# Performance work log

Hardware: AMD Instinct MI355X
Metric: run time of the kernel (lower is better)

Reference implementation:

```python
import jax, jax.numpy as jnp
import numpy as np

HEADS = 8


def setup_inputs() -> dict:
    key = jax.random.key(0)
    ks = jax.random.split(key, 6)
    dim = 256
    s = 0.02
    return {
        "x": jax.random.normal(ks[0], (8, dim, 32, 32), jnp.float32),
        "w_qkv": jax.random.normal(ks[1], (3 * dim, dim), jnp.float32) * s,
        "w_out": jax.random.normal(ks[2], (dim, dim), jnp.float32) * s,
        "b_out": jnp.zeros((dim,), jnp.float32),
        "w_g1": jax.random.normal(ks[3], (dim // 4, dim), jnp.float32) * s,
        "b_g1": jnp.zeros((dim // 4,), jnp.float32),
        "w_g2": jax.random.normal(ks[4], (1, dim // 4), jnp.float32) * s,
        "b_g2": jnp.zeros((1,), jnp.float32),
    }


def _conv1x1(t, w, bias=None):
    # 1x1 conv == channel matmul
    y = jnp.einsum('bchw,oc->bohw', t, w)
    if bias is not None:
        y = y + bias[None, :, None, None]
    return y


def _forward(x, w_qkv, w_out, b_out, w_g1, b_g1, w_g2, b_g2):
    b, c, h, w = x.shape
    heads = HEADS
    d = c // heads
    n = h * w
    m = min(h, w)
    scale = d ** (-0.5)

    qkv = _conv1x1(x, w_qkv)  # [b, 3c, h, w]

    def to_heads(t):  # 'b (h d) x y -> b h (x y) d'
        return t.reshape(b, heads, d, n).transpose(0, 1, 3, 2)

    q, k, v = (to_heads(t) for t in jnp.split(qkv, 3, axis=1))

    attn = jax.nn.softmax(jnp.einsum('bhid,bhjd->bhij', q, k) * scale, axis=-1)

    # diagonal branch (anti-diagonal scores are computed in the original but
    # never used in the output -> omitted as dead code)
    q2d = q.reshape(b, heads, h, w, d)
    k2d = k.reshape(b, heads, h, w, d)
    q_dm = jnp.diagonal(q2d, axis1=2, axis2=3)  # [b, heads, d, m]
    k_dm = jnp.diagonal(k2d, axis1=2, axis2=3)
    diag_main = jnp.einsum('bhnd,bhmd->bhnm', q_dm, k_dm) * scale  # [b, heads, d, d]
    diag_vec = jnp.diagonal(diag_main.mean(axis=1), axis1=-2, axis2=-1)  # [b, d]
    diag_vec = jnp.pad(diag_vec, ((0, 0), (0, n - m)))  # [b, n] (d == m)

    DIAG_WEIGHT = 0.3
    enhanced = attn + DIAG_WEIGHT * diag_vec[:, None, :, None]

    out = jnp.einsum('bhij,bhjd->bhid', enhanced, v)  # [b, heads, n, d]
    out = out.reshape(b, heads, h, w, d).transpose(0, 1, 4, 2, 3).reshape(b, c, h, w)

    # left/right asymmetry gate
    mid = w // 2
    left = x[:, :, :, :mid]
    right = x[:, :, :, mid:]
    asym = jnp.abs(left - right[:, :, :, ::-1])  # [b, c, h, w/2]
    # adaptive_avg_pool2d (h, w/2) -> (h, w) with even w == width repeat by 2
    pooled = jnp.repeat(asym, 2, axis=3)
    g = _conv1x1(pooled, w_g1, b_g1)
    g = jax.nn.gelu(g, approximate=False)
    g = jax.nn.sigmoid(_conv1x1(g, w_g2, b_g2))  # [b, 1, h, w]

    out = out * (1.0 + g)
    return _conv1x1(out, w_out, b_out)


def reference(x, w_qkv, w_out, b_out, w_g1, b_g1, w_g2, b_g2):
    return _forward(x, w_qkv, w_out, b_out, w_g1, b_g1, w_g2, b_g2)
```

## Files before the change

### kernel.cpp

```cpp
#include <hip/hip_runtime.h>
#include <hip/hip_bf16.h>
#include <math.h>

#define B 8
#define C 256
#define HEADS 8
#define D 32
#define NPIX 1024
#define OC 768
#define SCALE 0.17677669529663687f
#define LOG2E 1.4426950408889634f

typedef unsigned int uint;
typedef unsigned short u16;
typedef __attribute__((ext_vector_type(8))) short bf16x8;
typedef __attribute__((ext_vector_type(4))) short bf16x4;
typedef __attribute__((ext_vector_type(4))) float f32x4;

static __device__ inline u16 f2bf(float f) {
  uint u = __float_as_uint(f);
  return (u16)((u + 0x7fffu + ((u >> 16) & 1u)) >> 16);
}
static __device__ inline float bfval(u16 v) { return __uint_as_float((uint)v << 16); }
static __device__ inline float bf_lo(uint u) { return __uint_as_float(u << 16); }
static __device__ inline float bf_hi(uint u) { return __uint_as_float(u & 0xffff0000u); }

static __device__ inline uint pk2(float lo, float hi) {
  union { __hip_bfloat162 h; uint u; } cv;
  cv.h = __float22bfloat162_rn(float2{lo, hi});
  return cv.u;
}

__global__ __launch_bounds__(256) void k_prep_gate(
    const float* __restrict__ x, const float* __restrict__ wqkv,
    const float* __restrict__ wout,
    const float* __restrict__ wg1, const float* __restrict__ bg1,
    const float* __restrict__ wg2, const float* __restrict__ bg2,
    u16* __restrict__ WQ, u16* __restrict__ WO, u16* __restrict__ XT,
    float* __restrict__ gate) {
  const int bid = blockIdx.x, t = threadIdx.x;
  __shared__ float smem[16 * 257 + 16 * 65];
  if (bid < 256) {
    const float* src;
    u16* dst;
    int base;
    if (bid < 192) { src = wqkv; dst = WQ; base = bid * 1024; }
    else           { src = wout; dst = WO; base = (bid - 192) * 1024; }
    float4 v = *(const float4*)(src + base + t * 4);
    uint2 pk = make_uint2((uint)f2bf(v.x) | ((uint)f2bf(v.y) << 16),
                          (uint)f2bf(v.z) | ((uint)f2bf(v.w) << 16));
    *(uint2*)(dst + base + t * 4) = pk;
    return;
  }
  if (bid < 768) {
    u16 (*tile)[65] = (u16(*)[65])smem;
    const int id = bid - 256;
    const int pt = id & 15, ct = (id >> 4) & 3, b = id >> 6;
    {
      const int px = t & 63, cq = t >> 6;
      const float* xb = x + ((size_t)(b * C + ct * 64)) * NPIX + pt * 64;
#pragma unroll
      for (int m = 0; m < 16; ++m) {
        const int c = cq * 16 + m;
        tile[c][px] = f2bf(xb[(size_t)c * NPIX + px]);
      }
    }
    __syncthreads();
    {
      const int cc = t & 63, pq = t >> 6;
      const int c = ct * 64 + cc;
      const int kc = c >> 5, quad = (c >> 3) & 3, mm = c & 7;
      u16* dst = XT + ((size_t)((b * 64 + pt * 4 + pq) * 8 + kc) * 512 +
                       quad * 128 + mm);
#pragma unroll
      for (int m = 0; m < 16; ++m)
        dst[m * 8] = tile[cc][pq * 16 + m];
    }
    return;
  }
  const int id = bid - 768;
  const int h = id & 31, b = id >> 5;
  float* pl = smem;
  float* gl = smem + 16 * 257;
  {
    const int c = t;
    const float* row = x + ((size_t)(b * C + c) * NPIX + h * 32);
    float v[32];
#pragma unroll
    for (int m = 0; m < 32; ++m) v[m] = row[m];
#pragma unroll
    for (int k = 0; k < 16; ++k) pl[k * 257 + c] = fabsf(v[k] - v[31 - k]);
  }
  __syncthreads();

  const int o16 = t >> 4, k = t & 15;
#pragma unroll 1
  for (int p = 0; p < 4; ++p) {
    const int o = p * 16 + o16;
    const float* wr = wg1 + o * C;
    float a0 = 0.f, a1 = 0.f, a2 = 0.f, a3 = 0.f;
#pragma unroll 4
    for (int c = 0; c < C; c += 4) {
      a0 += wr[c]     * pl[k * 257 + c];
      a1 += wr[c + 1] * pl[k * 257 + c + 1];
      a2 += wr[c + 2] * pl[k * 257 + c + 2];
      a3 += wr[c + 3] * pl[k * 257 + c + 3];
    }
    float a = bg1[o] + ((a0 + a1) + (a2 + a3));
    gl[k * 65 + o] = 0.5f * a * (1.f + erff(a * 0.70710678118654752f));
  }
  __syncthreads();

  if (t < 16) {
    float s = bg2[0];
    for (int o = 0; o < 64; ++o)
      s += wg2[o] * gl[t * 65 + o];
    gate[(b * 32 + h) * 16 + t] = 1.f / (1.f + expf(-s));
  }
}

__global__ __launch_bounds__(256) void k_qkv_mfma(
    const u16* __restrict__ XTF, const u16* __restrict__ WQ,
    u16* __restrict__ Q, u16* __restrict__ Kk, u16* __restrict__ VT) {
  const int ob = blockIdx.x, pb = blockIdx.y, b = blockIdx.z;
  const int wv = threadIdx.x >> 6, lane = threadIdx.x & 63;
  const int quad = lane >> 4, l15 = lane & 15;
  const int part = ob >> 2;
  const int odl = (ob & 3) * 64 + wv * 16;
  const int hh = odl >> 5, d0 = odl & 31;
  const int bh = b * HEADS + hh;
  const int pix0 = pb * 128;

  const u16* arow = WQ + (size_t)(ob * 64 + wv * 16 + l15) * C;
  bf16x8 af[8];
#pragma unroll
  for (int kc = 0; kc < 8; ++kc)
    af[kc] = *(const bf16x8*)(arow + kc * 32 + quad * 8);

  const u16* xb = XTF + (size_t)(b * 64 + pb * 8) * 8 * 512 + lane * 8;
  f32x4 acc[8];
#pragma unroll
  for (int nt = 0; nt < 8; ++nt) acc[nt] = (f32x4){0.f, 0.f, 0.f, 0.f};

  for (int kc = 0; kc < 8; ++kc) {
#pragma unroll
    for (int nt = 0; nt < 8; ++nt) {
      bf16x8 bfr = *(const bf16x8*)(xb + (size_t)(nt * 8 + kc) * 512);
      acc[nt] = __builtin_amdgcn_mfma_f32_16x16x32_bf16(af[kc], bfr, acc[nt], 0, 0, 0);
    }
  }

  if (part == 0) {
    const float qs = SCALE * LOG2E;
    u16* dst = Q + (size_t)bh * NPIX * D;
#pragma unroll
    for (int nt = 0; nt < 8; ++nt) {
      const int pix = pix0 + nt * 16 + l15;
      uint2 pk = make_uint2(
          (uint)f2bf(acc[nt][0] * qs) | ((uint)f2bf(acc[nt][1] * qs) << 16),
          (uint)f2bf(acc[nt][2] * qs) | ((uint)f2bf(acc[nt][3] * qs) << 16));
      *(uint2*)(dst + (size_t)pix * D + d0 + 4 * quad) = pk;
    }
  } else if (part == 1) {
    u16* kfb = Kk + (size_t)bh * NPIX * D;
    const int lane_k8 = (((d0 >> 3) + (quad >> 1)) * 16 + l15) * 8 + (quad & 1) * 4;
#pragma unroll
    for (int nt = 0; nt < 8; ++nt) {
      uint2 pk = make_uint2(
          (uint)f2bf(acc[nt][0]) | ((uint)f2bf(acc[nt][1]) << 16),
          (uint)f2bf(acc[nt][2]) | ((uint)f2bf(acc[nt][3]) << 16));
      *(uint2*)(kfb + (size_t)(pb * 8 + nt) * 512 + lane_k8) = pk;
    }
  } else {
    u16* vb = VT + (size_t)bh * NPIX * D;
#pragma unroll
    for (int nt = 0; nt < 8; ++nt) {
      const int pix = pix0 + nt * 16 + l15;
      const int jb16 = pix >> 4, qa = (pix >> 2) & 3, m = pix & 3;
#pragma unroll
      for (int r = 0; r < 4; ++r) {
        const int d = d0 + 4 * quad + r;
        const int nta = d >> 4, l15a = d & 15;
        vb[((size_t)(jb16 * 2 + nta) * 64 + qa * 16 + l15a) * 4 + m] =
            f2bf(acc[nt][r]);
      }
    }
  }
}

__global__ __launch_bounds__(256) void k_red(
    const u16* __restrict__ Q, const u16* __restrict__ KF,
    const u16* __restrict__ VT, float* __restrict__ diagv,
    float* __restrict__ colsum) {
  const int bid = blockIdx.x, tid = threadIdx.x;
  __shared__ float red[256];
  if (bid < 8) {
    const int b = bid;
    const int hh = tid >> 5, dd = tid & 31;
    const u16* qb = Q + (size_t)(b * HEADS + hh) * NPIX * D;
    const u16* kb = KF + (size_t)(b * HEADS + hh) * NPIX * D;
    float s = 0.f;
#pragma unroll 4
    for (int t = 0; t < 32; ++t) {
      const int j = t * 33;
      float qv = bfval(qb[(size_t)j * D + dd]);
      float kv = bfval(kb[(size_t)(j >> 4) * 512 +
                          ((dd >> 3) * 16 + (j & 15)) * 8 + (dd & 7)]);
      s += qv * kv;
    }
    red[tid] = s;
    __syncthreads();
    if (tid < 32) {
      float v = 0.f;
#pragma unroll
      for (int h8 = 0; h8 < 8; ++h8) v += red[h8 * 32 + tid];
      diagv[b * 32 + tid] = v * (0.125f / LOG2E);
    }
  } else {
    const int bh = bid - 8;
    const int d = tid >> 3, sl = tid & 7;
    const int nta = d >> 4, l15a = d & 15;
    const u16* vb = VT + (size_t)bh * NPIX * D;
    float s = 0.f;
    for (int jb = 0; jb < 8; ++jb) {
      const int jb16 = sl * 8 + jb;
#pragma unroll
      for (int qa = 0; qa < 4; ++qa) {
        const uint2 u = *(const uint2*)(
            vb + ((size_t)(jb16 * 2 + nta) * 64 + qa * 16 + l15a) * 4);
        s += bf_lo(u.x) + bf_hi(u.x) + bf_lo(u.y) + bf_hi(u.y);
      }
    }
    red[tid] = s;
    __syncthreads();
    if (tid < 32) {
      float v = 0.f;
#pragma unroll
      for (int g = 0; g < 8; ++g) v += red[tid * 8 + g];
      colsum[bh * D + tid] = v;
    }
  }
}

__global__ __launch_bounds__(512, 4) void k_attn(
    const u16* __restrict__ Q, const u16* __restrict__ KF,
    const u16* __restrict__ VF, const float* __restrict__ diagv,
    const float* __restrict__ colsum, u16* __restrict__ AOT) {
  const int qc = blockIdx.x;
  const int bh = blockIdx.y;
  const int b = bh >> 3, hh = bh & 7;
  const int wv = threadIdx.x >> 6, lane = threadIdx.x & 63;
  const int quad = lane >> 4, l15 = lane & 15;
  const int i0 = qc * 128 + wv * 16;

  __shared__ u16 sbuf[2][4096];

  const u16* Qb  = Q  + (size_t)bh * NPIX * D;
  const u16* KFb = KF + (size_t)bh * NPIX * D;
  const u16* VFb = VF + (size_t)bh * NPIX * D;

  bf16x8 qfrag = *(const bf16x8*)(Qb + (size_t)(i0 + l15) * D + quad * 8);

  f32x4 oacc[2];
  oacc[0] = (f32x4){0.f, 0.f, 0.f, 0.f};
  oacc[1] = (f32x4){0.f, 0.f, 0.f, 0.f};
  float lacc[4] = {};

  const int soff = (wv >= 4 ? 2048 : 0) + (wv & 3) * 512 + lane * 8;
  const u16* gsrc = (wv < 4 ? KFb : VFb) + (wv & 3) * 512 + lane * 8;
  u16* ldst[2] = { &sbuf[0][soff], &sbuf[1][soff] };

  *(uint4*)(ldst[0]) = *(const uint4*)(gsrc);
  __syncthreads();

  int cur = 0;
  for (int it = 0; it < 16; ++it) {
    if (it < 15)
      *(uint4*)(ldst[cur ^ 1]) = *(const uint4*)(gsrc + (size_t)(it + 1) * 2048);
    const u16* sK = &sbuf[cur][0];
    const u16* sV = &sbuf[cur][2048];

    f32x4 st[4];
#pragma unroll
    for (int jt = 0; jt < 4; ++jt) {
      bf16x8 kfrag = *(const bf16x8*)(sK + jt * 512 + lane * 8);
      st[jt] = __builtin_amdgcn_mfma_f32_16x16x32_bf16(
          kfrag, qfrag, (f32x4){0.f, 0.f, 0.f, 0.f}, 0, 0, 0);
    }

#pragma unroll
    for (int jt = 0; jt < 4; ++jt)
#pragma unroll
      for (int r = 0; r < 4; ++r) {
        float pv = exp2f(fminf(st[jt][r], 80.f));
        lacc[r] += pv;
        st[jt][r] = pv;
      }

    __builtin_amdgcn_s_setprio(1);
#pragma unroll
    for (int jt = 0; jt < 4; ++jt) {
      union { uint u[2]; bf16x4 v; } pa;
      pa.u[0] = pk2(st[jt][0], st[jt][1]);
      pa.u[1] = pk2(st[jt][2], st[jt][3]);
#pragma unroll
      for (int nt = 0; nt < 2; ++nt) {
        bf16x4 vfr = *(const bf16x4*)(sV + (jt * 2 + nt) * 256 + lane * 4);
        oacc[nt] = __builtin_amdgcn_mfma_f32_16x16x16bf16_1k(
            pa.v, vfr, oacc[nt], 0, 0, 0);
      }
    }
    __builtin_amdgcn_s_setprio(0);

    __syncthreads();
    cur ^= 1;
  }

  float lt = (lacc[0] + lacc[1]) + (lacc[2] + lacc[3]);
  lt += __shfl_xor(lt, 16, 64);
  lt += __shfl_xor(lt, 32, 64);
  const float linv = 1.f / lt;
  float rinv[4];
#pragma unroll
  for (int r = 0; r < 4; ++r) rinv[r] = __shfl(linv, quad * 4 + r, 64);

  const bool do_diag = (i0 < 32);
  const int p16 = i0 >> 4;
  u16* aobase = AOT + ((size_t)(b * 64 + p16) * 8 + hh) * 512 + (l15 & 7);
  const int hi8 = l15 >> 3;
#pragma unroll
  for (int nt = 0; nt < 2; ++nt) {
    const int qa = nt * 2 + hi8;
    float cs = do_diag ? colsum[bh * D + (nt * 16 + l15)] : 0.f;
#pragma unroll
    for (int r = 0; r < 4; ++r) {
      const int irow = i0 + quad * 4 + r;
      float o = oacc[nt][r] * rinv[r];
      if (do_diag) o += 0.3f * diagv[b * 32 + irow] * cs;
      aobase[(qa * 16 + quad * 4 + r) * 8] = f2bf(o);
    }
  }
}

__global__ __launch_bounds__(256) void k_out_mfma(
    const u16* __restrict__ AOF, const u16* __restrict__ WO,
    const float* __restrict__ bout, const float* __restrict__ gate,
    float* __restrict__ out) {
  const int ob = blockIdx.x, pb = blockIdx.y, b = blockIdx.z;
  const int wv = threadIdx.x >> 6, lane = threadIdx.x & 63;
  const int quad = lane >> 4, l15 = lane & 15;
  const int o0 = ob * 64 + wv * 16;
  const int pix0 = pb * 128;

  const u16* arow = WO + (size_t)(o0 + l15) * C;
  bf16x8 af[8];
#pragma unroll
  for (int kc = 0; kc < 8; ++kc)
    af[kc] = *(const bf16x8*)(arow + kc * 32 + quad * 8);

  const u16* ab = AOF + (size_t)(b * 64 + pb * 8) * 8 * 512 + lane * 8;
  f32x4 acc[8];
#pragma unroll
  for (int nt = 0; nt < 8; ++nt) acc[nt] = (f32x4){0.f, 0.f, 0.f, 0.f};

  for (int kc = 0; kc < 8; ++kc) {
#pragma unroll
    for (int nt = 0; nt < 8; ++nt) {
      bf16x8 bfr = *(const bf16x8*)(ab + (size_t)(nt * 8 + kc) * 512);
      acc[nt] = __builtin_amdgcn_mfma_f32_16x16x32_bf16(af[kc], bfr, acc[nt], 0, 0, 0);
    }
  }

#pragma unroll
  for (int nt = 0; nt < 8; ++nt) {
    const int pix = pix0 + nt * 16 + l15;
    const float gf = 1.f + gate[(b * 32 + (pix >> 5)) * 16 + ((pix & 31) >> 1)];
#pragma unroll
    for (int r = 0; r < 4; ++r) {
      const int o = o0 + 4 * quad + r;
      out[((size_t)b * C + o) * NPIX + pix] = acc[nt][r] * gf + bout[o];
    }
  }
}

extern "C" void kernel_launch(void* const* d_in, const int* in_sizes, int n_in,
                              void* d_out, int out_size, void* d_ws, size_t ws_size,
                              hipStream_t stream) {
  const float* x    = (const float*)d_in[0];
  const float* wqkv = (const float*)d_in[1];
  const float* wout = (const float*)d_in[2];
  const float* bout = (const float*)d_in[3];
  const float* wg1  = (const float*)d_in[4];
  const float* bg1  = (const float*)d_in[5];
  const float* wg2  = (const float*)d_in[6];
  const float* bg2  = (const float*)d_in[7];
  float* out = (float*)d_out;

  const size_t SZ = (size_t)B * HEADS * NPIX * D;
  u16* XT = (u16*)d_ws;
  u16* WQ = XT + SZ;
  u16* WO = WQ + (size_t)OC * C;
  u16* Q  = WO + (size_t)C * C;
  u16* Kq = Q + SZ;
  u16* VT = Kq + SZ;
  float* DIAG = (float*)(VT + SZ);
  float* COL  = DIAG + 256;
  float* GATE = COL + 2048;
  u16* AOT = XT;

  hipLaunchKernelGGL(k_prep_gate, dim3(1024), dim3(256), 0, stream,
                     x, wqkv, wout, wg1, bg1, wg2, bg2, WQ, WO, XT, GATE);
  hipLaunchKernelGGL(k_qkv_mfma, dim3(12, 8, B), dim3(256), 0, stream,
                     XT, WQ, Q, Kq, VT);
  hipLaunchKernelGGL(k_red, dim3(72), dim3(256), 0, stream,
                     Q, Kq, VT, DIAG, COL);
  hipLaunchKernelGGL(k_attn, dim3(8, 64), dim3(512), 0, stream,
                     Q, Kq, VT, DIAG, COL, AOT);
  hipLaunchKernelGGL(k_out_mfma, dim3(4, 8, B), dim3(256), 0, stream,
                     AOT, WO, bout, GATE, out);
}
```

Before: 147.8 us.

## Stage QKV activations through double-buffered LDS and defer attention prefetch stores

The QKV projection kernel now cooperatively loads each k-chunk of the activation tile into a double-buffered shared memory buffer, prefetching the next chunk into registers while MFMAs run. Before, every wave re-read the same activation data from global memory. The attention kernel now holds its next K/V tile in registers and writes it to LDS after the compute, so the global load latency overlaps the MFMA work. The cost is a __syncthreads per k-chunk in the QKV kernel and extra register pressure in both kernels.

```diff
diff --git a/kernel.cpp b/kernel.cpp
--- a/kernel.cpp
+++ b/kernel.cpp
@@ -123,7 +123,8 @@
     const u16* __restrict__ XTF, const u16* __restrict__ WQ,
     u16* __restrict__ Q, u16* __restrict__ Kk, u16* __restrict__ VT) {
   const int ob = blockIdx.x, pb = blockIdx.y, b = blockIdx.z;
-  const int wv = threadIdx.x >> 6, lane = threadIdx.x & 63;
+  const int t = threadIdx.x;
+  const int wv = t >> 6, lane = t & 63;
   const int quad = lane >> 4, l15 = lane & 15;
   const int part = ob >> 2;
   const int odl = (ob & 3) * 64 + wv * 16;
@@ -131,23 +132,52 @@
   const int bh = b * HEADS + hh;
   const int pix0 = pb * 128;
 
+  __shared__ u16 sb[2][4096];
+
   const u16* arow = WQ + (size_t)(ob * 64 + wv * 16 + l15) * C;
   bf16x8 af[8];
 #pragma unroll
   for (int kc = 0; kc < 8; ++kc)
     af[kc] = *(const bf16x8*)(arow + kc * 32 + quad * 8);
 
-  const u16* xb = XTF + (size_t)(b * 64 + pb * 8) * 8 * 512 + lane * 8;
+  const u16* xb = XTF + (size_t)(b * 64 + pb * 8) * 8 * 512;
+  const int snt = t >> 5, si = (t & 31) * 16;
+
   f32x4 acc[8];
 #pragma unroll
   for (int nt = 0; nt < 8; ++nt) acc[nt] = (f32x4){0.f, 0.f, 0.f, 0.f};
 
+  {
+    const u16* p = xb + (size_t)(snt * 8 + 0) * 512 + si;
+    uint4 r0 = *(const uint4*)(p);
+    uint4 r1 = *(const uint4*)(p + 8);
+    u16* d = &sb[0][snt * 512 + si];
+    *(uint4*)(d) = r0;
+    *(uint4*)(d + 8) = r1;
+  }
+  __syncthreads();
+
+  int cur = 0;
   for (int kc = 0; kc < 8; ++kc) {
+    uint4 r0, r1;
+    if (kc < 7) {
+      const u16* p = xb + (size_t)(snt * 8 + kc + 1) * 512 + si;
+      r0 = *(const uint4*)(p);
+      r1 = *(const uint4*)(p + 8);
+    }
+    const u16* s = &sb[cur][0];
 #pragma unroll
     for (int nt = 0; nt < 8; ++nt) {
-      bf16x8 bfr = *(const bf16x8*)(xb + (size_t)(nt * 8 + kc) * 512);
+      bf16x8 bfr = *(const bf16x8*)(s + nt * 512 + lane * 8);
       acc[nt] = __builtin_amdgcn_mfma_f32_16x16x32_bf16(af[kc], bfr, acc[nt], 0, 0, 0);
     }
+    if (kc < 7) {
+      u16* d = &sb[cur ^ 1][snt * 512 + si];
+      *(uint4*)(d) = r0;
+      *(uint4*)(d + 8) = r1;
+    }
+    __syncthreads();
+    cur ^= 1;
   }
 
   if (part == 0) {
@@ -268,17 +298,19 @@
 
   const int soff = (wv >= 4 ? 2048 : 0) + (wv & 3) * 512 + lane * 8;
   const u16* gsrc = (wv < 4 ? KFb : VFb) + (wv & 3) * 512 + lane * 8;
-  u16* ldst[2] = { &sbuf[0][soff], &sbuf[1][soff] };
-
-  *(uint4*)(ldst[0]) = *(const uint4*)(gsrc);
+  u16* ldst0 = &sbuf[0][soff];
+  u16* ldst1 = &sbuf[1][soff];
+
+  *(uint4*)(ldst0) = *(const uint4*)(gsrc);
   __syncthreads();
 
   int cur = 0;
   for (int it = 0; it < 16; ++it) {
+    uint4 pre;
     if (it < 15)
-      *(uint4*)(ldst[cur ^ 1]) = *(const uint4*)(gsrc + (size_t)(it + 1) * 2048);
-    const u16* sK = &sbuf[cur][0];
-    const u16* sV = &sbuf[cur][2048];
+      pre = *(const uint4*)(gsrc + (size_t)(it + 1) * 2048);
+    const u16* sK = cur ? &sbuf[1][0] : &sbuf[0][0];
+    const u16* sV = sK + 2048;
 
     f32x4 st[4];
 #pragma unroll
@@ -312,6 +344,8 @@
     }
     __builtin_amdgcn_s_setprio(0);
 
+    if (it < 15)
+      *(uint4*)(cur ? ldst0 : ldst1) = pre;
     __syncthreads();
     cur ^= 1;
   }
```

New measurement: 144.8 us. -2.0%, faster.
